# Kernel tuning notes

Hardware: AMD Instinct MI355X
Metric: run time of the kernel (lower is better)

Reference implementation:

```python
import jax, jax.numpy as jnp
import numpy as np

N_NODES = 30000
DIM = 128
N_T = 6
N_EDGES = 480000
NEG_SLOPE = 0.2  # GATConv default leaky_relu slope


def _gat(x, src, dst, W, att_src, att_dst, b):
    # PyG GATConv, heads=1, add_self_loops=True, eval mode (no dropout).
    n = x.shape[0]
    loops = jnp.arange(n)
    src = jnp.concatenate([src, loops])
    dst = jnp.concatenate([dst, loops])
    h = x @ W                              # [N, D]
    a_s = h @ att_src                      # [N]
    a_d = h @ att_dst                      # [N]
    e = jax.nn.leaky_relu(a_s[src] + a_d[dst], NEG_SLOPE)   # [E+N]
    m = jax.ops.segment_max(e, dst, num_segments=n)
    ex = jnp.exp(e - m[dst])
    denom = jax.ops.segment_sum(ex, dst, num_segments=n)
    alpha = ex / denom[dst]
    out = jax.ops.segment_sum(h[src] * alpha[:, None], dst, num_segments=n)
    return out + b


def _sage(x, src, dst, Wl, bl, Wr, br):
    # PyG SAGEConv, mean aggregation, root_weight=True.
    n = x.shape[0]
    agg = jax.ops.segment_sum(x[src], dst, num_segments=n)
    cnt = jax.ops.segment_sum(jnp.ones_like(src, dtype=x.dtype), dst, num_segments=n)
    mean = agg / jnp.maximum(cnt, 1.0)[:, None]
    return mean @ Wl + bl + x @ Wr + br


def setup_inputs() -> dict:
    key = jax.random.key(0)
    ks = jax.random.split(key, 16)
    sc = 0.1
    inp = {
        "s": jax.random.randint(ks[0], (1024,), 0, N_NODES),
        "t_s": jax.random.randint(ks[1], (1024,), 0, N_T),
        "t_e": jax.random.randint(ks[2], (1024,), 0, N_T),
        "edge_index": jax.random.randint(ks[3], (N_T, 3, 2, N_EDGES), 0, N_NODES),
        "embed_weight": jax.random.normal(ks[4], (N_NODES, DIM), jnp.float32),
        "W_p": jax.random.normal(ks[5], (DIM, DIM), jnp.float32) * sc,
        "att_src_p": jax.random.normal(ks[6], (DIM,), jnp.float32) * sc,
        "att_dst_p": jax.random.normal(ks[7], (DIM,), jnp.float32) * sc,
        "b_p": jnp.zeros((DIM,), jnp.float32),
        "W_c": jax.random.normal(ks[8], (DIM, DIM), jnp.float32) * sc,
        "att_src_c": jax.random.normal(ks[9], (DIM,), jnp.float32) * sc,
        "att_dst_c": jax.random.normal(ks[10], (DIM,), jnp.float32) * sc,
        "b_c": jnp.zeros((DIM,), jnp.float32),
        "W_l": jax.random.normal(ks[11], (DIM, DIM), jnp.float32) * sc,
        "b_l": jnp.zeros((DIM,), jnp.float32),
        "W_r": jax.random.normal(ks[12], (DIM, DIM), jnp.float32) * sc,
        "b_r": jnp.zeros((DIM,), jnp.float32),
    }
    return inp


def reference(s, t_s, t_e, edge_index, embed_weight,
              W_p, att_src_p, att_dst_p, b_p,
              W_c, att_src_c, att_dst_c, b_c,
              W_l, b_l, W_r, b_r):
    outs = []
    for t in range(N_T):  # fixed small number of timesteps
        ei = edge_index[t]
        gp = _gat(embed_weight, ei[0, 0], ei[0, 1], W_p, att_src_p, att_dst_p, b_p)
        gc = _gat(embed_weight, ei[1, 0], ei[1, 1], W_c, att_src_c, att_dst_c, b_c)
        sg = _sage(embed_weight, ei[2, 0], ei[2, 1], W_l, b_l, W_r, b_r)
        outs.append((gp + gc + sg) / 3.0)  # HeteroConv aggr='mean'
    skill_embs = jnp.stack(outs)           # [n, N, D]
    return skill_embs[:, s, :]             # [n, |s|, D]
```

## Files before the change

### kernel.cpp

```cpp
#include <hip/hip_runtime.h>
#include <hip/hip_bf16.h>

#define NN 30000
#define DIM 128
#define NT 6
#define NE 480000
#define NSLOT 1024
#define NSEG (NT*3*NSLOT)
#define SEGCAP 96
#define NBM ((NN+31)/32)
#define QCAP 2048
#define HB 2048
#define NBUILD 2124
#define NCAST 876
#define NAGG (NSEG/16)

typedef __attribute__((ext_vector_type(8))) short bf16x8;
typedef __attribute__((ext_vector_type(4))) float f32x4;

__device__ __forceinline__ float lrelu(float x){ return x > 0.f ? x : 0.2f*x; }
__device__ __forceinline__ unsigned short f2b(float f){
    unsigned u = __float_as_uint(f);
    u = (u + 0x7FFFu + ((u>>16)&1u)) >> 16;
    return (unsigned short)u;
}
__device__ __forceinline__ float b2f(unsigned short b){
    return __uint_as_float(((unsigned)b)<<16);
}
__device__ __forceinline__ float blo(unsigned p){ return b2f((unsigned short)(p & 0xFFFF)); }
__device__ __forceinline__ float bhi(unsigned p){ return b2f((unsigned short)(p >> 16)); }
__device__ __forceinline__ unsigned hsh(int v){ return ((unsigned)v*2654435761u >> 21) & (HB-1); }

__global__ void k_prep(const float* __restrict__ Wp, const float* __restrict__ Wc,
        const float* __restrict__ Wl, const float* __restrict__ Wr,
        const float* __restrict__ aspv, const float* __restrict__ adpv,
        const float* __restrict__ ascv, const float* __restrict__ adcv,
        const int* __restrict__ s, unsigned* __restrict__ bm,
        unsigned* __restrict__ hmap, int* __restrict__ rep, int* __restrict__ cnt,
        float* __restrict__ wa, unsigned short* __restrict__ WT4){
    int m = blockIdx.x, t = threadIdx.x;
    if (m >= 5){
        int b = m - 5;
        int per = (NSEG + 7)/8;
        for (int j = b*per + t; j < (b+1)*per && j < NSEG; j += 256) cnt[j] = 0;
        return;
    }
    if (m == 4){
        __shared__ int hk[HB];
        __shared__ int hv[HB];
        __shared__ unsigned bms[NBM];
        for (int j = t; j < HB; j += 256){ hk[j] = -1; hv[j] = 1<<30; }
        for (int j = t; j < NBM; j += 256) bms[j] = 0u;
        __syncthreads();
        for (int i = t; i < NSLOT; i += 256){
            int v = s[i];
            unsigned idx = hsh(v);
            while (true){
                int old = atomicCAS(&hk[idx], -1, v);
                if (old == -1 || old == v){ atomicMin(&hv[idx], i); break; }
                idx = (idx+1)&(HB-1);
            }
            atomicOr(&bms[v>>5], 1u << (v&31));
        }
        __syncthreads();
        for (int j = t; j < NBM; j += 256) bm[j] = bms[j];
        for (int j = t; j < HB; j += 256){
            int k = hk[j];
            hmap[j] = (k < 0) ? 0xFFFFFFFFu : (((unsigned)k << 10) | (unsigned)hv[j]);
        }
        for (int i = t; i < NSLOT; i += 256){
            int v = s[i];
            unsigned idx = hsh(v);
            while (hk[idx] != v) idx = (idx+1)&(HB-1);
            rep[i] = hv[idx];
        }
        return;
    }
    const float* W = (m==0) ? Wp : (m==1) ? Wc : (m==2) ? Wl : Wr;
    unsigned short* WT = WT4 + (size_t)m*DIM*DIM;
    if (m < 2 && t < DIM){
        const float* avs = m ? ascv : aspv;
        const float* avd = m ? adcv : adpv;
        float* wab = wa + m*2*DIM;
        float sv = 0.f, dv = 0.f;
        for (int n = 0; n < DIM; n++){
            float w = W[t*DIM + n];
            sv += w*avs[n]; dv += w*avd[n];
        }
        wab[t] = sv; wab[DIM + t] = dv;
    }
    for (int j = t; j < DIM*DIM; j += blockDim.x){
        int n = j >> 7, k = j & 127;
        WT[n*DIM + k] = f2b(W[k*DIM + n]);
    }
}

__global__ __launch_bounds__(256) void k_castbuild(
        const float* __restrict__ X, const float* __restrict__ wa,
        unsigned* __restrict__ Xbf,
        float* __restrict__ asp, float* __restrict__ adp,
        float* __restrict__ asc, float* __restrict__ adc,
        const int* __restrict__ EI,
        const unsigned* __restrict__ bm, const unsigned* __restrict__ hmap,
        int* __restrict__ cnt, int* __restrict__ csr){
    __shared__ unsigned bms[NBM];
    __shared__ unsigned q[QCAP];
    __shared__ int qn;
    int bx = blockIdx.x;
    int lane = threadIdx.x & 63;
    int wib = threadIdx.x >> 6;
    if (bx < NCAST){
        for (int node = bx*4 + wib; node < NN; node += NCAST*4){
            float2 x = *(const float2*)&X[(size_t)node*DIM + lane*2];
            Xbf[(size_t)node*64 + lane] = (unsigned)f2b(x.x) | ((unsigned)f2b(x.y) << 16);
            float sp = x.x*wa[2*lane]     + x.y*wa[2*lane+1];
            float dp = x.x*wa[128+2*lane] + x.y*wa[128+2*lane+1];
            float sc = x.x*wa[256+2*lane] + x.y*wa[256+2*lane+1];
            float dc = x.x*wa[384+2*lane] + x.y*wa[384+2*lane+1];
            #pragma unroll
            for (int off = 32; off; off >>= 1){
                sp += __shfl_xor(sp, off); dp += __shfl_xor(dp, off);
                sc += __shfl_xor(sc, off); dc += __shfl_xor(dc, off);
            }
            if (lane == 0){ asp[node]=sp; adp[node]=dp; asc[node]=sc; adc[node]=dc; }
        }
        return;
    }
    int bb = bx - NCAST;
    int row = bb / 118, bxx = bb - row*118;
    for (int j = threadIdx.x; j < NBM; j += 256) bms[j] = bm[j];
    if (threadIdx.x == 0) qn = 0;
    __syncthreads();
    const int Q = NE/4;
    const int G = 118*256;
    const int4* dstp = (const int4*)(EI + (size_t)(2*row+1)*NE);
    const int4* srcp = (const int4*)(EI + (size_t)(2*row)*NE);
    int tid = bxx*256 + threadIdx.x;

    int4 d[4]; int ix[4]; bool va[4];
    #pragma unroll
    for (int u = 0; u < 4; u++){
        ix[u] = tid + u*G;
        va[u] = ix[u] < Q;
        d[u] = va[u] ? dstp[ix[u]] : make_int4(0,0,0,0);
    }
    unsigned mk[4];
    #pragma unroll
    for (int u = 0; u < 4; u++){
        unsigned m0 = va[u] ? ((bms[d[u].x>>5] >> (d[u].x&31)) & 1u) : 0u;
        unsigned m1 = va[u] ? ((bms[d[u].y>>5] >> (d[u].y&31)) & 1u) : 0u;
        unsigned m2 = va[u] ? ((bms[d[u].z>>5] >> (d[u].z&31)) & 1u) : 0u;
        unsigned m3 = va[u] ? ((bms[d[u].w>>5] >> (d[u].w&31)) & 1u) : 0u;
        mk[u] = m0 | (m1<<1) | (m2<<2) | (m3<<3);
    }
    int4 sv[4];
    #pragma unroll
    for (int u = 0; u < 4; u++)
        if (mk[u]) sv[u] = srcp[ix[u]];
    #pragma unroll
    for (int u = 0; u < 4; u++){
        #pragma unroll
        for (int c = 0; c < 4; c++){
            bool p = (mk[u] >> c) & 1u;
            unsigned long long bal = __ballot(p);
            if (bal){
                int cntw = __popcll(bal);
                int base = 0;
                if (lane == 0) base = atomicAdd(&qn, cntw);
                base = __shfl(base, 0);
                if (p){
                    int dv = (c==0)?d[u].x:(c==1)?d[u].y:(c==2)?d[u].z:d[u].w;
                    int so = (c==0)?sv[u].x:(c==1)?sv[u].y:(c==2)?sv[u].z:sv[u].w;
                    int pos = base + __popcll(bal & ((1ull<<lane)-1ull));
                    if (pos < QCAP) q[pos] = ((unsigned)dv<<15) | (unsigned)so;
                }
            }
        }
    }
    __syncthreads();
    int base = row*NSLOT;
    int tot = qn; if (tot > QCAP) tot = QCAP;
    for (int j = threadIdx.x; j < tot; j += 256){
        unsigned e = q[j];
        int dst = (int)(e >> 15);
        int src = (int)(e & 32767u);
        unsigned idx = hsh(dst);
        unsigned he;
        while (((he = hmap[idx]) >> 10) != (unsigned)dst) idx = (idx+1)&(HB-1);
        int sl = (int)(he & 1023u);
        int p = atomicAdd(&cnt[base+sl], 1);
        if (p < SEGCAP) csr[(size_t)(base+sl)*SEGCAP + p] = src;
    }
}

__global__ __launch_bounds__(256) void k_aggemm(const unsigned* __restrict__ Xbf,
        const float* __restrict__ asp, const float* __restrict__ adp,
        const float* __restrict__ asc, const float* __restrict__ adc,
        const int* __restrict__ s, const int* __restrict__ cnt, const int* __restrict__ csr,
        const unsigned short* __restrict__ WT4,
        float* __restrict__ aggOut, float* __restrict__ xWr){
    __shared__ unsigned tile[16][72];
    int bx = blockIdx.x;
    int lane = threadIdx.x & 63;
    int wib = threadIdx.x >> 6;
    if (bx >= NAGG){
        int blk = bx - NAGG;
        const unsigned short* WT = WT4 + (size_t)3*DIM*DIM;
        int r0 = blk*64 + wib*16;
        int ar = r0 + (lane & 15); if (ar > NSLOT-1) ar = NSLOT-1;
        int g4 = lane >> 4;
        const unsigned short* Arow = (const unsigned short*)(Xbf + (size_t)s[ar]*64);
        bf16x8 Af[4];
        #pragma unroll
        for (int ks = 0; ks < 4; ks++)
            Af[ks] = *(const bf16x8*)&Arow[ks*32 + g4*8];
        int cl = lane & 15;
        #pragma unroll
        for (int ct = 0; ct < 8; ct++){
            f32x4 acc = {0.f,0.f,0.f,0.f};
            int bcol = ct*16 + cl;
            #pragma unroll
            for (int ks = 0; ks < 4; ks++){
                bf16x8 bF = *(const bf16x8*)&WT[bcol*DIM + ks*32 + g4*8];
                acc = __builtin_amdgcn_mfma_f32_16x16x32_bf16(Af[ks], bF, acc, 0, 0, 0);
            }
            #pragma unroll
            for (int r = 0; r < 4; r++){
                int rw = r0 + g4*4 + r;
                if (rw < NSLOT) xWr[(size_t)rw*DIM + bcol] = acc[r];
            }
        }
        return;
    }
    int base_gw = bx*16;
    int tg = base_gw >> 10;
    int g = tg % 3;
    const float* as = (g==1) ? asc : asp;
    const float* ad = (g==1) ? adc : adp;
    for (int k = 0; k < 4; k++){
        int segi = wib*4 + k;
        int gw = base_gw + segi;
        int slot = gw & (NSLOT-1);
        int n = cnt[gw]; if (n > SEGCAP) n = SEGCAP;
        const int* lst = csr + (size_t)gw*SEGCAP;
        int src0 = (lane < n) ? lst[lane] : 0;
        int src1 = (64+lane < n) ? lst[64+lane] : 0;
        int n0 = n < 64 ? n : 64;
        float w0, w1, wself = 0.f, scale;
        int v = -1;
        if (g == 2){
            w0 = (lane < n) ? 1.f : 0.f;
            w1 = (64+lane < n) ? 1.f : 0.f;
            scale = 1.f / (float)(n > 0 ? n : 1);
        } else {
            v = s[slot];
            float adv = ad[v];
            float eself = lrelu(as[v] + adv);
            float e0 = (lane < n)    ? lrelu(as[src0]+adv) : -3e38f;
            float e1 = (64+lane < n) ? lrelu(as[src1]+adv) : -3e38f;
            float m = fmaxf(eself, fmaxf(e0, e1));
            #pragma unroll
            for (int off = 32; off; off >>= 1) m = fmaxf(m, __shfl_xor(m, off));
            w0 = (lane < n)    ? __expf(e0 - m) : 0.f;
            w1 = (64+lane < n) ? __expf(e1 - m) : 0.f;
            float ds = w0 + w1;
            #pragma unroll
            for (int off = 32; off; off >>= 1) ds += __shfl_xor(ds, off);
            wself = __expf(eself - m);
            scale = 1.f / (wself + ds);
        }
        float a0 = 0.f, a1 = 0.f;
        int j = 0;
        for (; j+7 < n0; j += 8){
            int   si[8]; float qi[8]; unsigned ki[8];
            #pragma unroll
            for (int u = 0; u < 8; u++){ si[u] = __shfl(src0, j+u); qi[u] = __shfl(w0, j+u); }
            #pragma unroll
            for (int u = 0; u < 8; u++) ki[u] = Xbf[(size_t)si[u]*64 + lane];
            #pragma unroll
            for (int u = 0; u < 8; u++){ a0 += qi[u]*blo(ki[u]); a1 += qi[u]*bhi(ki[u]); }
        }
        for (; j+3 < n0; j += 4){
            int s0=__shfl(src0,j), s1=__shfl(src0,j+1), s2=__shfl(src0,j+2), s3=__shfl(src0,j+3);
            float q0=__shfl(w0,j), q1=__shfl(w0,j+1), q2=__shfl(w0,j+2), q3=__shfl(w0,j+3);
            unsigned k0=Xbf[(size_t)s0*64+lane];
            unsigned k1=Xbf[(size_t)s1*64+lane];
            unsigned k2=Xbf[(size_t)s2*64+lane];
            unsigned k3=Xbf[(size_t)s3*64+lane];
            a0 += q0*blo(k0) + q1*blo(k1) + q2*blo(k2) + q3*blo(k3);
            a1 += q0*bhi(k0) + q1*bhi(k1) + q2*bhi(k2) + q3*bhi(k3);
        }
        for (; j < n0; j++){
            int sj=__shfl(src0,j);
            float qj=__shfl(w0,j);
            unsigned pk=Xbf[(size_t)sj*64+lane];
            a0 += qj*blo(pk); a1 += qj*bhi(pk);
        }
        for (j = 64; j < n; j++){
            int sj=__shfl(src1,j-64);
            float qj=__shfl(w1,j-64);
            unsigned pk=Xbf[(size_t)sj*64+lane];
            a0 += qj*blo(pk); a1 += qj*bhi(pk);
        }
        if (g < 2){
            unsigned pk = Xbf[(size_t)v*64 + lane];
            a0 += wself*blo(pk); a1 += wself*bhi(pk);
        }
        tile[segi][lane] = (unsigned)f2b(a0*scale) | ((unsigned)f2b(a1*scale) << 16);
    }
    __syncthreads();
    const unsigned short* WT = WT4 + (size_t)g*DIM*DIM;
    int r = lane & 15, g4 = lane >> 4;
    bf16x8 Af[4];
    #pragma unroll
    for (int ks = 0; ks < 4; ks++)
        Af[ks] = *(const bf16x8*)&tile[r][ks*16 + g4*4];
    #pragma unroll
    for (int ct = 0; ct < 2; ct++){
        f32x4 acc = {0.f,0.f,0.f,0.f};
        int bcol = wib*32 + ct*16 + r;
        #pragma unroll
        for (int ks = 0; ks < 4; ks++){
            bf16x8 bF = *(const bf16x8*)&WT[bcol*DIM + ks*32 + g4*8];
            acc = __builtin_amdgcn_mfma_f32_16x16x32_bf16(Af[ks], bF, acc, 0, 0, 0);
        }
        #pragma unroll
        for (int rr = 0; rr < 4; rr++){
            int segrow = g4*4 + rr;
            aggOut[(size_t)(base_gw + segrow)*DIM + bcol] = acc[rr];
        }
    }
}

__global__ void k_gather(const int* __restrict__ rep,
                         const float* __restrict__ aggOut, const float* __restrict__ xWr,
                         const float* __restrict__ bp, const float* __restrict__ bc,
                         const float* __restrict__ bl, const float* __restrict__ br,
                         float* __restrict__ out){
    int i = blockIdx.x*blockDim.x + threadIdx.x;
    if (i >= NT*NSLOT*DIM) return;
    int d = i & 127;
    int r = (i >> 7) & (NSLOT-1);
    int t = i >> 17;
    int rp = rep[r];
    size_t base = ((size_t)(t*3)*NSLOT + rp)*DIM + d;
    out[i] = (aggOut[base] + aggOut[base + NSLOT*DIM] + aggOut[base + 2*NSLOT*DIM]
              + xWr[(size_t)rp*DIM + d]
              + bp[d] + bc[d] + bl[d] + br[d]) * (1.f/3.f);
}

extern "C" void kernel_launch(void* const* d_in, const int* in_sizes, int n_in,
                              void* d_out, int out_size, void* d_ws, size_t ws_size,
                              hipStream_t stream) {
    const int*   s    = (const int*)d_in[0];
    const int*   EI   = (const int*)d_in[3];
    const float* X    = (const float*)d_in[4];
    const float* Wp   = (const float*)d_in[5];
    const float* aspv = (const float*)d_in[6];
    const float* adpv = (const float*)d_in[7];
    const float* bp   = (const float*)d_in[8];
    const float* Wc   = (const float*)d_in[9];
    const float* ascv = (const float*)d_in[10];
    const float* adcv = (const float*)d_in[11];
    const float* bc   = (const float*)d_in[12];
    const float* Wl   = (const float*)d_in[13];
    const float* bl   = (const float*)d_in[14];
    const float* Wr   = (const float*)d_in[15];
    const float* br   = (const float*)d_in[16];
    float* out = (float*)d_out;

    char* w = (char*)d_ws;
    unsigned* Xbf = (unsigned*)w; w += (size_t)NN*64*4;
    unsigned short* WT4 = (unsigned short*)w; w += (size_t)4*DIM*DIM*2;
    float* wa  = (float*)w; w += (size_t)4*DIM*4;
    float* asp = (float*)w; w += (size_t)NN*4;
    float* adp = (float*)w; w += (size_t)NN*4;
    float* asc = (float*)w; w += (size_t)NN*4;
    float* adc = (float*)w; w += (size_t)NN*4;
    unsigned* bm = (unsigned*)w; w += (size_t)((NBM+3)&~3)*4;
    unsigned* hmap = (unsigned*)w; w += (size_t)HB*4;
    int* rep  = (int*)w; w += (size_t)NSLOT*4;
    int* cnt  = (int*)w; w += (size_t)NSEG*4;
    int* csr  = (int*)w; w += (size_t)NSEG*SEGCAP*4;
    float* aggOut = (float*)w; w += (size_t)NSEG*DIM*4;
    float* xWr = (float*)w; w += (size_t)NSLOT*DIM*4;

    k_prep      <<<13, 256, 0, stream>>>(Wp, Wc, Wl, Wr, aspv, adpv, ascv, adcv,
                                         s, bm, hmap, rep, cnt, wa, WT4);
    k_castbuild <<<NCAST+NBUILD, 256, 0, stream>>>(X, wa, Xbf, asp, adp, asc, adc,
                                                   EI, bm, hmap, cnt, csr);
    k_aggemm    <<<NAGG+16, 256, 0, stream>>>(Xbf, asp, adp, asc, adc, s, cnt, csr,
                                              WT4, aggOut, xWr);
    k_gather    <<<NT*NSLOT*DIM/256, 256, 0, stream>>>(rep, aggOut, xWr, bp, bc, bl, br, out);
}
```

Measured before the change: 75.43 us.

## Fuse three-relation GEMMs, root projection and bias into one finalize kernel

Each block now aggregates all three relations for 8 slots of one timestep and accumulates their projections plus the root-weight projection of the self node in a single MFMA accumulator chain. Bias sums are precomputed in the prep kernel. The per-relation aggOut and xWr buffers are replaced by one fused fin buffer, so the gather only copies rows. The cost is half-utilised MFMA tiles, since only 8 of 16 rows are valid, and the root projection is recomputed per timestep.

```diff
diff --git a/kernel.cpp b/kernel.cpp
--- a/kernel.cpp
+++ b/kernel.cpp
@@ -11,9 +11,8 @@
 #define NBM ((NN+31)/32)
 #define QCAP 2048
 #define HB 2048
+#define NCAST 876
 #define NBUILD 2124
-#define NCAST 876
-#define NAGG (NSEG/16)
 
 typedef __attribute__((ext_vector_type(8))) short bf16x8;
 typedef __attribute__((ext_vector_type(4))) float f32x4;
@@ -35,9 +34,12 @@
         const float* __restrict__ Wl, const float* __restrict__ Wr,
         const float* __restrict__ aspv, const float* __restrict__ adpv,
         const float* __restrict__ ascv, const float* __restrict__ adcv,
+        const float* __restrict__ bp, const float* __restrict__ bc,
+        const float* __restrict__ bl, const float* __restrict__ br,
         const int* __restrict__ s, unsigned* __restrict__ bm,
         unsigned* __restrict__ hmap, int* __restrict__ rep, int* __restrict__ cnt,
-        float* __restrict__ wa, unsigned short* __restrict__ WT4){
+        float* __restrict__ wa, float* __restrict__ bsum,
+        unsigned short* __restrict__ WT4){
     int m = blockIdx.x, t = threadIdx.x;
     if (m >= 5){
         int b = m - 5;
@@ -78,6 +80,7 @@
     }
     const float* W = (m==0) ? Wp : (m==1) ? Wc : (m==2) ? Wl : Wr;
     unsigned short* WT = WT4 + (size_t)m*DIM*DIM;
+    if (m == 0 && t < DIM) bsum[t] = bp[t] + bc[t] + bl[t] + br[t];
     if (m < 2 && t < DIM){
         const float* avs = m ? ascv : aspv;
         const float* avd = m ? adcv : adpv;
@@ -193,54 +196,23 @@
     }
 }
 
-__global__ __launch_bounds__(256) void k_aggemm(const unsigned* __restrict__ Xbf,
+__global__ __launch_bounds__(256) void k_aggfin(const unsigned* __restrict__ Xbf,
         const float* __restrict__ asp, const float* __restrict__ adp,
         const float* __restrict__ asc, const float* __restrict__ adc,
         const int* __restrict__ s, const int* __restrict__ cnt, const int* __restrict__ csr,
-        const unsigned short* __restrict__ WT4,
-        float* __restrict__ aggOut, float* __restrict__ xWr){
-    __shared__ unsigned tile[16][72];
-    int bx = blockIdx.x;
+        const unsigned short* __restrict__ WT4, const float* __restrict__ bsum,
+        float* __restrict__ fin){
+    __shared__ unsigned tile[3][8][72];
+    int b = blockIdx.x;
+    int t = b >> 7, sblk = b & 127;
+    int slot0 = sblk*8;
     int lane = threadIdx.x & 63;
     int wib = threadIdx.x >> 6;
-    if (bx >= NAGG){
-        int blk = bx - NAGG;
-        const unsigned short* WT = WT4 + (size_t)3*DIM*DIM;
-        int r0 = blk*64 + wib*16;
-        int ar = r0 + (lane & 15); if (ar > NSLOT-1) ar = NSLOT-1;
-        int g4 = lane >> 4;
-        const unsigned short* Arow = (const unsigned short*)(Xbf + (size_t)s[ar]*64);
-        bf16x8 Af[4];
-        #pragma unroll
-        for (int ks = 0; ks < 4; ks++)
-            Af[ks] = *(const bf16x8*)&Arow[ks*32 + g4*8];
-        int cl = lane & 15;
-        #pragma unroll
-        for (int ct = 0; ct < 8; ct++){
-            f32x4 acc = {0.f,0.f,0.f,0.f};
-            int bcol = ct*16 + cl;
-            #pragma unroll
-            for (int ks = 0; ks < 4; ks++){
-                bf16x8 bF = *(const bf16x8*)&WT[bcol*DIM + ks*32 + g4*8];
-                acc = __builtin_amdgcn_mfma_f32_16x16x32_bf16(Af[ks], bF, acc, 0, 0, 0);
-            }
-            #pragma unroll
-            for (int r = 0; r < 4; r++){
-                int rw = r0 + g4*4 + r;
-                if (rw < NSLOT) xWr[(size_t)rw*DIM + bcol] = acc[r];
-            }
-        }
-        return;
-    }
-    int base_gw = bx*16;
-    int tg = base_gw >> 10;
-    int g = tg % 3;
-    const float* as = (g==1) ? asc : asp;
-    const float* ad = (g==1) ? adc : adp;
-    for (int k = 0; k < 4; k++){
-        int segi = wib*4 + k;
-        int gw = base_gw + segi;
-        int slot = gw & (NSLOT-1);
+    for (int qq = 0; qq < 6; qq++){
+        int ls = wib*6 + qq;
+        int g = ls >> 3, sl = ls & 7;
+        int slot = slot0 + sl;
+        int gw = (t*3+g)*NSLOT + slot;
         int n = cnt[gw]; if (n > SEGCAP) n = SEGCAP;
         const int* lst = csr + (size_t)gw*SEGCAP;
         int src0 = (lane < n) ? lst[lane] : 0;
@@ -253,6 +225,8 @@
             w1 = (64+lane < n) ? 1.f : 0.f;
             scale = 1.f / (float)(n > 0 ? n : 1);
         } else {
+            const float* as = g ? asc : asp;
+            const float* ad = g ? adc : adp;
             v = s[slot];
             float adv = ad[v];
             float eself = lrelu(as[v] + adv);
@@ -306,36 +280,43 @@
             unsigned pk = Xbf[(size_t)v*64 + lane];
             a0 += wself*blo(pk); a1 += wself*bhi(pk);
         }
-        tile[segi][lane] = (unsigned)f2b(a0*scale) | ((unsigned)f2b(a1*scale) << 16);
+        tile[g][sl][lane] = (unsigned)f2b(a0*scale) | ((unsigned)f2b(a1*scale) << 16);
     }
     __syncthreads();
-    const unsigned short* WT = WT4 + (size_t)g*DIM*DIM;
     int r = lane & 15, g4 = lane >> 4;
-    bf16x8 Af[4];
-    #pragma unroll
-    for (int ks = 0; ks < 4; ks++)
-        Af[ks] = *(const bf16x8*)&tile[r][ks*16 + g4*4];
+    int rs = r & 7;
+    int selfnode = s[slot0 + rs];
+    const unsigned short* Arow = (const unsigned short*)(Xbf + (size_t)selfnode*64);
     #pragma unroll
     for (int ct = 0; ct < 2; ct++){
         f32x4 acc = {0.f,0.f,0.f,0.f};
         int bcol = wib*32 + ct*16 + r;
         #pragma unroll
+        for (int mm = 0; mm < 3; mm++){
+            #pragma unroll
+            for (int ks = 0; ks < 4; ks++){
+                bf16x8 af = *(const bf16x8*)&tile[mm][rs][ks*16 + g4*4];
+                bf16x8 bF = *(const bf16x8*)&WT4[(size_t)mm*DIM*DIM + bcol*DIM + ks*32 + g4*8];
+                acc = __builtin_amdgcn_mfma_f32_16x16x32_bf16(af, bF, acc, 0, 0, 0);
+            }
+        }
+        #pragma unroll
         for (int ks = 0; ks < 4; ks++){
-            bf16x8 bF = *(const bf16x8*)&WT[bcol*DIM + ks*32 + g4*8];
-            acc = __builtin_amdgcn_mfma_f32_16x16x32_bf16(Af[ks], bF, acc, 0, 0, 0);
-        }
+            bf16x8 af = *(const bf16x8*)&Arow[ks*32 + g4*8];
+            bf16x8 bF = *(const bf16x8*)&WT4[(size_t)3*DIM*DIM + bcol*DIM + ks*32 + g4*8];
+            acc = __builtin_amdgcn_mfma_f32_16x16x32_bf16(af, bF, acc, 0, 0, 0);
+        }
+        float bs = bsum[bcol];
         #pragma unroll
         for (int rr = 0; rr < 4; rr++){
             int segrow = g4*4 + rr;
-            aggOut[(size_t)(base_gw + segrow)*DIM + bcol] = acc[rr];
-        }
-    }
-}
-
-__global__ void k_gather(const int* __restrict__ rep,
-                         const float* __restrict__ aggOut, const float* __restrict__ xWr,
-                         const float* __restrict__ bp, const float* __restrict__ bc,
-                         const float* __restrict__ bl, const float* __restrict__ br,
+            if (segrow < 8)
+                fin[(size_t)(t*NSLOT + slot0 + segrow)*DIM + bcol] = (acc[rr] + bs) * (1.f/3.f);
+        }
+    }
+}
+
+__global__ void k_gather(const int* __restrict__ rep, const float* __restrict__ fin,
                          float* __restrict__ out){
     int i = blockIdx.x*blockDim.x + threadIdx.x;
     if (i >= NT*NSLOT*DIM) return;
@@ -343,10 +324,7 @@
     int r = (i >> 7) & (NSLOT-1);
     int t = i >> 17;
     int rp = rep[r];
-    size_t base = ((size_t)(t*3)*NSLOT + rp)*DIM + d;
-    out[i] = (aggOut[base] + aggOut[base + NSLOT*DIM] + aggOut[base + 2*NSLOT*DIM]
-              + xWr[(size_t)rp*DIM + d]
-              + bp[d] + bc[d] + bl[d] + br[d]) * (1.f/3.f);
+    out[i] = fin[(size_t)(t*NSLOT + rp)*DIM + d];
 }
 
 extern "C" void kernel_launch(void* const* d_in, const int* in_sizes, int n_in,
@@ -373,6 +351,7 @@
     unsigned* Xbf = (unsigned*)w; w += (size_t)NN*64*4;
     unsigned short* WT4 = (unsigned short*)w; w += (size_t)4*DIM*DIM*2;
     float* wa  = (float*)w; w += (size_t)4*DIM*4;
+    float* bsum = (float*)w; w += (size_t)DIM*4;
     float* asp = (float*)w; w += (size_t)NN*4;
     float* adp = (float*)w; w += (size_t)NN*4;
     float* asc = (float*)w; w += (size_t)NN*4;
@@ -382,14 +361,14 @@
     int* rep  = (int*)w; w += (size_t)NSLOT*4;
     int* cnt  = (int*)w; w += (size_t)NSEG*4;
     int* csr  = (int*)w; w += (size_t)NSEG*SEGCAP*4;
-    float* aggOut = (float*)w; w += (size_t)NSEG*DIM*4;
-    float* xWr = (float*)w; w += (size_t)NSLOT*DIM*4;
+    float* fin = (float*)w; w += (size_t)NT*NSLOT*DIM*4;
 
     k_prep      <<<13, 256, 0, stream>>>(Wp, Wc, Wl, Wr, aspv, adpv, ascv, adcv,
-                                         s, bm, hmap, rep, cnt, wa, WT4);
+                                         bp, bc, bl, br,
+                                         s, bm, hmap, rep, cnt, wa, bsum, WT4);
     k_castbuild <<<NCAST+NBUILD, 256, 0, stream>>>(X, wa, Xbf, asp, adp, asc, adc,
                                                    EI, bm, hmap, cnt, csr);
-    k_aggemm    <<<NAGG+16, 256, 0, stream>>>(Xbf, asp, adp, asc, adc, s, cnt, csr,
-                                              WT4, aggOut, xWr);
-    k_gather    <<<NT*NSLOT*DIM/256, 256, 0, stream>>>(rep, aggOut, xWr, bp, bc, bl, br, out);
-}
+    k_aggfin    <<<NT*128, 256, 0, stream>>>(Xbf, asp, adp, asc, adc, s, cnt, csr,
+                                             WT4, bsum, fin);
+    k_gather    <<<NT*NSLOT*DIM/256, 256, 0, stream>>>(rep, fin, out);
+}
```

After: 85.73 us. 1.14x slower.
